# Kernel optimization log

Hardware: AMD Instinct MI355X
Metric: run time of the kernel (lower is better)

Reference implementation:

```python
import jax, jax.numpy as jnp
import numpy as np

D_K = 1024
HEADS = 16
HK = 64
HV = 64


def setup_inputs() -> dict:
    key = jax.random.key(0)
    ks = jax.random.split(key, 12)
    B, S = 4, 2048
    sc_in = 1.0 / np.sqrt(D_K)
    sc_u = 1.0 / np.sqrt(HV * HEADS)
    return {
        "q": jax.random.normal(ks[0], (B, S, D_K), jnp.float32),
        "k": jax.random.normal(ks[1], (B, S, D_K), jnp.float32),
        "v": jax.random.normal(ks[2], (B, S, D_K), jnp.float32),
        "Wq": jax.random.normal(ks[3], (D_K, HK * HEADS), jnp.float32) * sc_in,
        "bq": jax.random.normal(ks[4], (HK * HEADS,), jnp.float32) * sc_in,
        "Wk": jax.random.normal(ks[5], (D_K, HK * HEADS), jnp.float32) * sc_in,
        "bk": jax.random.normal(ks[6], (HK * HEADS,), jnp.float32) * sc_in,
        "Wv": jax.random.normal(ks[7], (D_K, HV * HEADS), jnp.float32) * sc_in,
        "bv": jax.random.normal(ks[8], (HV * HEADS,), jnp.float32) * sc_in,
        "Wu": jax.random.normal(ks[9], (HV * HEADS, D_K), jnp.float32) * sc_u,
        "bu": jax.random.normal(ks[10], (D_K,), jnp.float32) * sc_u,
    }


def reference(q, k, v, Wq, bq, Wk, bk, Wv, bv, Wu, bu):
    B, S, _ = q.shape
    # QKV projections, split heads: (B, S, H, dh) -> (B, H, S, dh)
    qh = (q @ Wq + bq).reshape(B, S, HEADS, HK).transpose(0, 2, 1, 3)
    kh = (k @ Wk + bk).reshape(B, S, HEADS, HK).transpose(0, 2, 1, 3)
    vh = (v @ Wv + bv).reshape(B, S, HEADS, HV).transpose(0, 2, 1, 3)
    # Naive attention: scores scaled by sqrt(head_size) as in Sdpa
    scores = jnp.einsum("bhqd,bhkd->bhqk", qh, kh) / jnp.sqrt(
        jnp.asarray(HK, qh.dtype)
    )
    attn = jax.nn.softmax(scores, axis=-1)
    out = jnp.einsum("bhqk,bhkd->bhqd", attn, vh)  # (B, H, S, HV)
    # Merge heads: (B, S, H*HV), then output projection
    merged = out.transpose(0, 2, 1, 3).reshape(B, S, HEADS * HV)
    return merged @ Wu + bu
```

## Files before the change

### kernel.cpp

```cpp
#include <hip/hip_runtime.h>

typedef __bf16 bf16;
typedef __bf16 bf16x8 __attribute__((ext_vector_type(8)));
typedef __bf16 bf16x4 __attribute__((ext_vector_type(4)));
typedef float  f32x4  __attribute__((ext_vector_type(4)));

#define GLD_LDS16(gp, lp) __builtin_amdgcn_global_load_lds( \
    (const __attribute__((address_space(1))) unsigned int*)(const void*)(gp), \
    (__attribute__((address_space(3))) unsigned int*)(void*)(lp), 16, 0, 0)

constexpr int BB = 4, SSEQ = 2048, DK = 1024, NH = 16, DH = 64;
constexpr int M = BB * SSEQ;

constexpr size_t SZ_X = (size_t)M * DK * 2;
constexpr size_t SZ_W = (size_t)DK * DK * 2;
constexpr size_t OFF_QBF = 0;
constexpr size_t OFF_KBF = OFF_QBF + SZ_X;
constexpr size_t OFF_VBF = OFF_KBF + SZ_X;
constexpr size_t OFF_WQT = OFF_VBF + SZ_X;
constexpr size_t OFF_WKT = OFF_WQT + SZ_W;
constexpr size_t OFF_WVT = OFF_WKT + SZ_W;
constexpr size_t OFF_WUT = OFF_WVT + SZ_W;
constexpr size_t OFF_QH  = OFF_WUT + SZ_W;
constexpr size_t OFF_KH  = OFF_QH + SZ_X;
constexpr size_t OFF_VTH = OFF_KH + SZ_X;
constexpr size_t OFF_MRG = OFF_VTH + SZ_X;

__global__ void cvt_x(const float* __restrict__ q, const float* __restrict__ k,
                      const float* __restrict__ v,
                      bf16* __restrict__ qb, bf16* __restrict__ kb, bf16* __restrict__ vb) {
    const float* s = (blockIdx.z == 0) ? q : (blockIdx.z == 1) ? k : v;
    bf16*        d = (blockIdx.z == 0) ? qb : (blockIdx.z == 1) ? kb : vb;
    size_t i = (size_t)blockIdx.x * blockDim.x + threadIdx.x;
    float4 val = ((const float4*)s)[i];
    bf16x4 o = { (bf16)val.x, (bf16)val.y, (bf16)val.z, (bf16)val.w };
    ((bf16x4*)d)[i] = o;
}

__global__ void cvt_wT(const float* __restrict__ wq, const float* __restrict__ wk,
                       const float* __restrict__ wv, const float* __restrict__ wu,
                       bf16* __restrict__ wqt, bf16* __restrict__ wkt,
                       bf16* __restrict__ wvt, bf16* __restrict__ wut) {
    const float* w = (blockIdx.z == 0) ? wq : (blockIdx.z == 1) ? wk
                   : (blockIdx.z == 2) ? wv : wu;
    bf16* o        = (blockIdx.z == 0) ? wqt : (blockIdx.z == 1) ? wkt
                   : (blockIdx.z == 2) ? wvt : wut;
    __shared__ float t[64][65];
    int tx = threadIdx.x & 63, ty = threadIdx.x >> 6;
    int bx = blockIdx.x * 64, by = blockIdx.y * 64;
#pragma unroll
    for (int r = 0; r < 16; r++) {
        int row = ty * 16 + r;
        t[row][tx] = w[(size_t)(by + row) * DK + bx + tx];
    }
    __syncthreads();
#pragma unroll
    for (int r = 0; r < 16; r++) {
        int row2 = ty * 16 + r;
        o[(size_t)(bx + row2) * DK + by + tx] = (bf16)t[tx][row2];
    }
}

struct GArg {
    const bf16* A; const bf16* BT; const float* bias; void* out; int mode; float oscale;
};

__global__ __launch_bounds__(256, 2) void gemm_bt(GArg g0, GArg g1, GArg g2) {
    GArg g;
    if (blockIdx.z == 0) g = g0; else if (blockIdx.z == 1) g = g1; else g = g2;
    __shared__ __attribute__((aligned(16))) bf16 As[128 * 32];
    __shared__ __attribute__((aligned(16))) bf16 Bs[128 * 32];
    const int tid = threadIdx.x;
    const int lane = tid & 63, wv = tid >> 6;
    const int wm = (wv & 1) * 64, wn = (wv >> 1) * 64;
    const int cl = lane & 15, qd = lane >> 4;
    const int rowbase = blockIdx.y * 128, colbase = blockIdx.x * 128;

    f32x4 acc[4][4];
#pragma unroll
    for (int i = 0; i < 4; i++)
#pragma unroll
        for (int j = 0; j < 4; j++) acc[i][j] = f32x4{0.f, 0.f, 0.f, 0.f};

    for (int k0 = 0; k0 < DK; k0 += 32) {
        __syncthreads();
#pragma unroll
        for (int c = 0; c < 2; c++) {
            int f = (c * 256 + tid) * 8;
            int row = f >> 5, col = f & 31;
            GLD_LDS16(g.A + (size_t)(rowbase + row) * DK + k0 + col, &As[f]);
        }
#pragma unroll
        for (int c = 0; c < 2; c++) {
            int f = (c * 256 + tid) * 8;
            int row = f >> 5, col = f & 31;
            GLD_LDS16(g.BT + (size_t)(colbase + row) * DK + k0 + col, &Bs[f]);
        }
        __syncthreads();
        bf16x8 af[4], bfr[4];
#pragma unroll
        for (int i = 0; i < 4; i++)
            af[i] = *(const bf16x8*)&As[(wm + i * 16 + cl) * 32 + qd * 8];
#pragma unroll
        for (int j = 0; j < 4; j++)
            bfr[j] = *(const bf16x8*)&Bs[(wn + j * 16 + cl) * 32 + qd * 8];
#pragma unroll
        for (int i = 0; i < 4; i++)
#pragma unroll
            for (int j = 0; j < 4; j++)
                acc[i][j] = __builtin_amdgcn_mfma_f32_16x16x32_bf16(af[i], bfr[j], acc[i][j], 0, 0, 0);
    }

    if (g.mode == 2) {
        float* out = (float*)g.out;
#pragma unroll
        for (int i = 0; i < 4; i++)
#pragma unroll
            for (int j = 0; j < 4; j++)
#pragma unroll
                for (int r = 0; r < 4; r++) {
                    int row = rowbase + wm + i * 16 + qd * 4 + r;
                    int col = colbase + wn + j * 16 + cl;
                    out[(size_t)row * DK + col] = (acc[i][j][r] + g.bias[col]) * g.oscale;
                }
    } else if (g.mode == 0) {
        bf16* out = (bf16*)g.out;
#pragma unroll
        for (int i = 0; i < 4; i++)
#pragma unroll
            for (int j = 0; j < 4; j++)
#pragma unroll
                for (int r = 0; r < 4; r++) {
                    int row = rowbase + wm + i * 16 + qd * 4 + r;
                    int col = colbase + wn + j * 16 + cl;
                    int b_ = row >> 11, s_ = row & 2047, h_ = col >> 6, d_ = col & 63;
                    float v = (acc[i][j][r] + g.bias[col]) * g.oscale;
                    out[(((size_t)(b_ * NH + h_)) * SSEQ + s_) * DH + d_] = (bf16)v;
                }
    } else {
        bf16* out = (bf16*)g.out;
#pragma unroll
        for (int i = 0; i < 4; i++)
#pragma unroll
            for (int j = 0; j < 4; j++)
#pragma unroll
                for (int r = 0; r < 4; r++) {
                    int row = rowbase + wm + i * 16 + qd * 4 + r;
                    int col = colbase + wn + j * 16 + cl;
                    int b_ = row >> 11, s_ = row & 2047, h_ = col >> 6, d_ = col & 63;
                    float v = (acc[i][j][r] + g.bias[col]) * g.oscale;
                    out[(((size_t)(b_ * NH + h_)) * DH + d_) * SSEQ + s_] = (bf16)v;
                }
    }
}

__global__ __launch_bounds__(256, 4) void attn(const bf16* __restrict__ Qh,
                                               const bf16* __restrict__ Kh,
                                               const bf16* __restrict__ VTh,
                                               bf16* __restrict__ mrg) {
    __shared__ __attribute__((aligned(16))) bf16 Ks[64 * 64];
    __shared__ __attribute__((aligned(16))) bf16 VTs[64 * 64];
    __shared__ __attribute__((aligned(16))) bf16 Pb[4][32 * 72];
    const int tid = threadIdx.x;
    const int lane = tid & 63, w = tid >> 6;
    const int cl = lane & 15, qd = lane >> 4;
    const int bh = blockIdx.y;
    const int qbase = blockIdx.x * 128;
    const bf16* Qb = Qh + (size_t)bh * SSEQ * DH;
    const bf16* Kb = Kh + (size_t)bh * SSEQ * DH;
    const bf16* Vb = VTh + (size_t)bh * DH * SSEQ;

    bf16x8 qf[2][2];
#pragma unroll
    for (int mi = 0; mi < 2; mi++) {
        int sq = qbase + w * 32 + mi * 16 + cl;
        qf[mi][0] = *(const bf16x8*)&Qb[(size_t)sq * DH + qd * 8];
        qf[mi][1] = *(const bf16x8*)&Qb[(size_t)sq * DH + 32 + qd * 8];
    }
    f32x4 O[2][4];
#pragma unroll
    for (int mi = 0; mi < 2; mi++)
#pragma unroll
        for (int jv = 0; jv < 4; jv++) O[mi][jv] = f32x4{0.f, 0.f, 0.f, 0.f};
    float ps[2][4];
#pragma unroll
    for (int mi = 0; mi < 2; mi++)
#pragma unroll
        for (int r = 0; r < 4; r++) ps[mi][r] = 0.f;

    for (int kt = 0; kt < 32; kt++) {
        const int kbase = kt * 64;
        __syncthreads();
#pragma unroll
        for (int c = 0; c < 2; c++) {
            int L = c * 256 + tid;
            int row = L >> 3, lc = (L & 7) ^ (row & 7);
            GLD_LDS16(Kb + (size_t)(kbase + row) * DH + lc * 8, &Ks[L * 8]);
        }
#pragma unroll
        for (int c = 0; c < 2; c++) {
            int L = c * 256 + tid;
            int row = L >> 3, lc = (L & 7) ^ (row & 7);
            GLD_LDS16(Vb + (size_t)row * SSEQ + kbase + lc * 8, &VTs[L * 8]);
        }
        __syncthreads();

#pragma unroll
        for (int mi = 0; mi < 2; mi++) {
            f32x4 Sc[4];
#pragma unroll
            for (int j = 0; j < 4; j++) Sc[j] = f32x4{0.f, 0.f, 0.f, 0.f};
#pragma unroll
            for (int kc = 0; kc < 2; kc++)
#pragma unroll
                for (int j = 0; j < 4; j++) {
                    bf16x8 bfr = *(const bf16x8*)&Ks[(j * 16 + cl) * 64 + (((kc * 4 + qd) ^ (cl & 7)) * 8)];
                    Sc[j] = __builtin_amdgcn_mfma_f32_16x16x32_bf16(qf[mi][kc], bfr, Sc[j], 0, 0, 0);
                }
#pragma unroll
            for (int j = 0; j < 4; j++)
#pragma unroll
                for (int r = 0; r < 4; r++) {
                    float p = __builtin_amdgcn_exp2f(Sc[j][r]);
                    ps[mi][r] += p;
                    Pb[w][(mi * 16 + qd * 4 + r) * 72 + j * 16 + cl] = (bf16)p;
                }
        }

#pragma unroll
        for (int kc = 0; kc < 2; kc++) {
            bf16x8 vf[4];
#pragma unroll
            for (int jv = 0; jv < 4; jv++)
                vf[jv] = *(const bf16x8*)&VTs[(jv * 16 + cl) * 64 + (((kc * 4 + qd) ^ (cl & 7)) * 8)];
#pragma unroll
            for (int mi = 0; mi < 2; mi++) {
                bf16x8 pf = *(const bf16x8*)&Pb[w][(mi * 16 + cl) * 72 + kc * 32 + qd * 8];
#pragma unroll
                for (int jv = 0; jv < 4; jv++)
                    O[mi][jv] = __builtin_amdgcn_mfma_f32_16x16x32_bf16(pf, vf[jv], O[mi][jv], 0, 0, 0);
            }
        }
    }

    int b_ = bh >> 4, h_ = bh & 15;
#pragma unroll
    for (int mi = 0; mi < 2; mi++)
#pragma unroll
        for (int r = 0; r < 4; r++) {
            float t = ps[mi][r];
#pragma unroll
            for (int off = 1; off < 16; off <<= 1) t += __shfl_xor(t, off);
            float inv = 1.0f / t;
            int sq = qbase + w * 32 + mi * 16 + qd * 4 + r;
            size_t rowoff = ((size_t)(b_ * SSEQ + sq)) * DK + h_ * DH;
#pragma unroll
            for (int jv = 0; jv < 4; jv++)
                mrg[rowoff + jv * 16 + cl] = (bf16)(O[mi][jv][r] * inv);
        }
}

extern "C" void kernel_launch(void* const* d_in, const int* in_sizes, int n_in,
                              void* d_out, int out_size, void* d_ws, size_t ws_size,
                              hipStream_t stream) {
    const float* q  = (const float*)d_in[0];
    const float* k  = (const float*)d_in[1];
    const float* v  = (const float*)d_in[2];
    const float* Wq = (const float*)d_in[3];
    const float* bq = (const float*)d_in[4];
    const float* Wk = (const float*)d_in[5];
    const float* bk = (const float*)d_in[6];
    const float* Wv = (const float*)d_in[7];
    const float* bv = (const float*)d_in[8];
    const float* Wu = (const float*)d_in[9];
    const float* bu = (const float*)d_in[10];
    char* ws = (char*)d_ws;
    bf16* qbf = (bf16*)(ws + OFF_QBF);
    bf16* kbf = (bf16*)(ws + OFF_KBF);
    bf16* vbf = (bf16*)(ws + OFF_VBF);
    bf16* wqt = (bf16*)(ws + OFF_WQT);
    bf16* wkt = (bf16*)(ws + OFF_WKT);
    bf16* wvt = (bf16*)(ws + OFF_WVT);
    bf16* wut = (bf16*)(ws + OFF_WUT);
    bf16* qh  = (bf16*)(ws + OFF_QH);
    bf16* kh  = (bf16*)(ws + OFF_KH);
    bf16* vth = (bf16*)(ws + OFF_VTH);
    bf16* mrg = (bf16*)(ws + OFF_MRG);

    cvt_x<<<dim3(8192, 1, 3), 256, 0, stream>>>(q, k, v, qbf, kbf, vbf);
    cvt_wT<<<dim3(16, 16, 4), 256, 0, stream>>>(Wq, Wk, Wv, Wu, wqt, wkt, wvt, wut);

    GArg gq{qbf, wqt, bq, (void*)qh, 0, 0.18033688011112043f};
    GArg gk{kbf, wkt, bk, (void*)kh, 0, 1.0f};
    GArg gv{vbf, wvt, bv, (void*)vth, 1, 1.0f};
    gemm_bt<<<dim3(8, 64, 3), 256, 0, stream>>>(gq, gk, gv);

    attn<<<dim3(16, 64), 256, 0, stream>>>(qh, kh, vth, mrg);

    GArg go{mrg, wut, bu, d_out, 2, 1.0f};
    gemm_bt<<<dim3(8, 64, 1), 256, 0, stream>>>(go, go, go);
}
```

Baseline: 376.4 us.

## Restructure attention to keep P in registers with double-buffered K/V tiles

The attention kernel now computes S transposed (K as the A operand), so the exponentiated probabilities land in the register layout the PV MFMA (16x16x16) needs, which removes the per-wave LDS round trip for P. Each block handles 256 queries (64 per wave) with double-buffered K/V LDS tiles prefetched one step ahead, and a flat grid remapped so the heads sharing a compute-die group are co-scheduled for L2 reuse. The Q/K projection GEMM writes plain row-major output, and the V projection swaps MFMA operands so the transposed store is more contiguous. In exchange, register pressure rises and occupancy drops to 2 blocks per CU.

```diff
diff --git a/kernel.cpp b/kernel.cpp
--- a/kernel.cpp
+++ b/kernel.cpp
@@ -4,10 +4,16 @@
 typedef __bf16 bf16x8 __attribute__((ext_vector_type(8)));
 typedef __bf16 bf16x4 __attribute__((ext_vector_type(4)));
 typedef float  f32x4  __attribute__((ext_vector_type(4)));
+typedef short  s16x4  __attribute__((ext_vector_type(4)));
 
 #define GLD_LDS16(gp, lp) __builtin_amdgcn_global_load_lds( \
     (const __attribute__((address_space(1))) unsigned int*)(const void*)(gp), \
     (__attribute__((address_space(3))) unsigned int*)(void*)(lp), 16, 0, 0)
+
+static __device__ __forceinline__ f32x4 mfma16(bf16x4 a, bf16x4 b, f32x4 c) {
+    return __builtin_amdgcn_mfma_f32_16x16x16bf16_1k(
+        __builtin_bit_cast(s16x4, a), __builtin_bit_cast(s16x4, b), c, 0, 0, 0);
+}
 
 constexpr int BB = 4, SSEQ = 2048, DK = 1024, NH = 16, DH = 64;
 constexpr int M = BB * SSEQ;
@@ -82,6 +88,7 @@
 #pragma unroll
         for (int j = 0; j < 4; j++) acc[i][j] = f32x4{0.f, 0.f, 0.f, 0.f};
 
+    const bool swapped = (g.mode == 1);
     for (int k0 = 0; k0 < DK; k0 += 32) {
         __syncthreads();
 #pragma unroll
@@ -104,11 +111,19 @@
 #pragma unroll
         for (int j = 0; j < 4; j++)
             bfr[j] = *(const bf16x8*)&Bs[(wn + j * 16 + cl) * 32 + qd * 8];
-#pragma unroll
-        for (int i = 0; i < 4; i++)
-#pragma unroll
-            for (int j = 0; j < 4; j++)
-                acc[i][j] = __builtin_amdgcn_mfma_f32_16x16x32_bf16(af[i], bfr[j], acc[i][j], 0, 0, 0);
+        if (swapped) {
+#pragma unroll
+            for (int i = 0; i < 4; i++)
+#pragma unroll
+                for (int j = 0; j < 4; j++)
+                    acc[i][j] = __builtin_amdgcn_mfma_f32_16x16x32_bf16(bfr[j], af[i], acc[i][j], 0, 0, 0);
+        } else {
+#pragma unroll
+            for (int i = 0; i < 4; i++)
+#pragma unroll
+                for (int j = 0; j < 4; j++)
+                    acc[i][j] = __builtin_amdgcn_mfma_f32_16x16x32_bf16(af[i], bfr[j], acc[i][j], 0, 0, 0);
+        }
     }
 
     if (g.mode == 2) {
@@ -133,9 +148,8 @@
                 for (int r = 0; r < 4; r++) {
                     int row = rowbase + wm + i * 16 + qd * 4 + r;
                     int col = colbase + wn + j * 16 + cl;
-                    int b_ = row >> 11, s_ = row & 2047, h_ = col >> 6, d_ = col & 63;
                     float v = (acc[i][j][r] + g.bias[col]) * g.oscale;
-                    out[(((size_t)(b_ * NH + h_)) * SSEQ + s_) * DH + d_] = (bf16)v;
+                    out[(size_t)row * DK + col] = (bf16)v;
                 }
     } else {
         bf16* out = (bf16*)g.out;
@@ -145,119 +159,121 @@
             for (int j = 0; j < 4; j++)
 #pragma unroll
                 for (int r = 0; r < 4; r++) {
-                    int row = rowbase + wm + i * 16 + qd * 4 + r;
-                    int col = colbase + wn + j * 16 + cl;
-                    int b_ = row >> 11, s_ = row & 2047, h_ = col >> 6, d_ = col & 63;
-                    float v = (acc[i][j][r] + g.bias[col]) * g.oscale;
-                    out[(((size_t)(b_ * NH + h_)) * DH + d_) * SSEQ + s_] = (bf16)v;
+                    int colg = colbase + wn + j * 16 + qd * 4 + r;
+                    int rowg = rowbase + wm + i * 16 + cl;
+                    int b_ = rowg >> 11, s_ = rowg & 2047;
+                    float v = (acc[i][j][r] + g.bias[colg]) * g.oscale;
+                    out[((size_t)(b_ * NH + (colg >> 6)) * DH + (colg & 63)) * SSEQ + s_] = (bf16)v;
                 }
     }
 }
 
-__global__ __launch_bounds__(256, 4) void attn(const bf16* __restrict__ Qh,
+__global__ __launch_bounds__(256, 2) void attn(const bf16* __restrict__ Qh,
                                                const bf16* __restrict__ Kh,
                                                const bf16* __restrict__ VTh,
                                                bf16* __restrict__ mrg) {
-    __shared__ __attribute__((aligned(16))) bf16 Ks[64 * 64];
-    __shared__ __attribute__((aligned(16))) bf16 VTs[64 * 64];
-    __shared__ __attribute__((aligned(16))) bf16 Pb[4][32 * 72];
+    __shared__ __attribute__((aligned(16))) bf16 Ks[2][64 * 64];
+    __shared__ __attribute__((aligned(16))) bf16 VTs[2][64 * 64];
     const int tid = threadIdx.x;
     const int lane = tid & 63, w = tid >> 6;
     const int cl = lane & 15, qd = lane >> 4;
-    const int bh = blockIdx.y;
-    const int qbase = blockIdx.x * 128;
-    const bf16* Qb = Qh + (size_t)bh * SSEQ * DH;
-    const bf16* Kb = Kh + (size_t)bh * SSEQ * DH;
+    const int F = blockIdx.x;
+    const int xcd = F & 7, slot = F >> 3;
+    const int bh = xcd * 8 + (slot & 7);
+    const int qt = slot >> 3;
+    const int b_ = bh >> 4, h_ = bh & 15;
+    const int qbase = qt * 256;
+    const bf16* Qb = Qh + ((size_t)b_ * SSEQ) * DK + h_ * DH;
+    const bf16* Kb = Kh + ((size_t)b_ * SSEQ) * DK + h_ * DH;
     const bf16* Vb = VTh + (size_t)bh * DH * SSEQ;
 
-    bf16x8 qf[2][2];
-#pragma unroll
-    for (int mi = 0; mi < 2; mi++) {
-        int sq = qbase + w * 32 + mi * 16 + cl;
-        qf[mi][0] = *(const bf16x8*)&Qb[(size_t)sq * DH + qd * 8];
-        qf[mi][1] = *(const bf16x8*)&Qb[(size_t)sq * DH + 32 + qd * 8];
-    }
-    f32x4 O[2][4];
-#pragma unroll
-    for (int mi = 0; mi < 2; mi++)
+    bf16x8 qf[4][2];
+#pragma unroll
+    for (int mi = 0; mi < 4; mi++) {
+        int q = qbase + w * 64 + mi * 16 + cl;
+        qf[mi][0] = *(const bf16x8*)&Qb[(size_t)q * DK + qd * 8];
+        qf[mi][1] = *(const bf16x8*)&Qb[(size_t)q * DK + 32 + qd * 8];
+    }
+    f32x4 O[4][4];
+#pragma unroll
+    for (int mi = 0; mi < 4; mi++)
 #pragma unroll
         for (int jv = 0; jv < 4; jv++) O[mi][jv] = f32x4{0.f, 0.f, 0.f, 0.f};
-    float ps[2][4];
-#pragma unroll
-    for (int mi = 0; mi < 2; mi++)
-#pragma unroll
-        for (int r = 0; r < 4; r++) ps[mi][r] = 0.f;
-
-    for (int kt = 0; kt < 32; kt++) {
-        const int kbase = kt * 64;
-        __syncthreads();
+    float ps[4] = {0.f, 0.f, 0.f, 0.f};
+
+    auto stage = [&](int kt, int buf) {
 #pragma unroll
         for (int c = 0; c < 2; c++) {
             int L = c * 256 + tid;
             int row = L >> 3, lc = (L & 7) ^ (row & 7);
-            GLD_LDS16(Kb + (size_t)(kbase + row) * DH + lc * 8, &Ks[L * 8]);
+            GLD_LDS16(Kb + (size_t)(kt * 64 + row) * DK + lc * 8, &Ks[buf][L * 8]);
         }
 #pragma unroll
         for (int c = 0; c < 2; c++) {
             int L = c * 256 + tid;
             int row = L >> 3, lc = (L & 7) ^ (row & 7);
-            GLD_LDS16(Vb + (size_t)row * SSEQ + kbase + lc * 8, &VTs[L * 8]);
-        }
+            GLD_LDS16(Vb + (size_t)row * SSEQ + kt * 64 + lc * 8, &VTs[buf][L * 8]);
+        }
+    };
+    stage(0, 0);
+
+    for (int kt = 0; kt < 32; kt++) {
+        const int buf = kt & 1;
         __syncthreads();
-
-#pragma unroll
-        for (int mi = 0; mi < 2; mi++) {
-            f32x4 Sc[4];
-#pragma unroll
-            for (int j = 0; j < 4; j++) Sc[j] = f32x4{0.f, 0.f, 0.f, 0.f};
-#pragma unroll
-            for (int kc = 0; kc < 2; kc++)
-#pragma unroll
-                for (int j = 0; j < 4; j++) {
-                    bf16x8 bfr = *(const bf16x8*)&Ks[(j * 16 + cl) * 64 + (((kc * 4 + qd) ^ (cl & 7)) * 8)];
-                    Sc[j] = __builtin_amdgcn_mfma_f32_16x16x32_bf16(qf[mi][kc], bfr, Sc[j], 0, 0, 0);
+        if (kt + 1 < 32) stage(kt + 1, buf ^ 1);
+
+        bf16x4 pf[4][4];
+#pragma unroll
+        for (int jt = 0; jt < 4; jt++) {
+            bf16x8 kf0 = *(const bf16x8*)&Ks[buf][(jt * 16 + cl) * 64 + ((qd ^ (cl & 7)) * 8)];
+            bf16x8 kf1 = *(const bf16x8*)&Ks[buf][(jt * 16 + cl) * 64 + (((4 + qd) ^ (cl & 7)) * 8)];
+#pragma unroll
+            for (int mi = 0; mi < 4; mi++) {
+                f32x4 S = __builtin_amdgcn_mfma_f32_16x16x32_bf16(kf0, qf[mi][0],
+                                                                  f32x4{0.f, 0.f, 0.f, 0.f}, 0, 0, 0);
+                S = __builtin_amdgcn_mfma_f32_16x16x32_bf16(kf1, qf[mi][1], S, 0, 0, 0);
+                bf16x4 p4;
+                float s = 0.f;
+#pragma unroll
+                for (int r = 0; r < 4; r++) {
+                    float p = __builtin_amdgcn_exp2f(S[r]);
+                    s += p;
+                    p4[r] = (bf16)p;
                 }
-#pragma unroll
-            for (int j = 0; j < 4; j++)
-#pragma unroll
-                for (int r = 0; r < 4; r++) {
-                    float p = __builtin_amdgcn_exp2f(Sc[j][r]);
-                    ps[mi][r] += p;
-                    Pb[w][(mi * 16 + qd * 4 + r) * 72 + j * 16 + cl] = (bf16)p;
-                }
-        }
-
-#pragma unroll
-        for (int kc = 0; kc < 2; kc++) {
-            bf16x8 vf[4];
-#pragma unroll
-            for (int jv = 0; jv < 4; jv++)
-                vf[jv] = *(const bf16x8*)&VTs[(jv * 16 + cl) * 64 + (((kc * 4 + qd) ^ (cl & 7)) * 8)];
-#pragma unroll
-            for (int mi = 0; mi < 2; mi++) {
-                bf16x8 pf = *(const bf16x8*)&Pb[w][(mi * 16 + cl) * 72 + kc * 32 + qd * 8];
-#pragma unroll
-                for (int jv = 0; jv < 4; jv++)
-                    O[mi][jv] = __builtin_amdgcn_mfma_f32_16x16x32_bf16(pf, vf[jv], O[mi][jv], 0, 0, 0);
+                ps[mi] += s;
+                pf[mi][jt] = p4;
             }
         }
-    }
-
-    int b_ = bh >> 4, h_ = bh & 15;
-#pragma unroll
-    for (int mi = 0; mi < 2; mi++)
-#pragma unroll
-        for (int r = 0; r < 4; r++) {
-            float t = ps[mi][r];
-#pragma unroll
-            for (int off = 1; off < 16; off <<= 1) t += __shfl_xor(t, off);
-            float inv = 1.0f / t;
-            int sq = qbase + w * 32 + mi * 16 + qd * 4 + r;
-            size_t rowoff = ((size_t)(b_ * SSEQ + sq)) * DK + h_ * DH;
-#pragma unroll
-            for (int jv = 0; jv < 4; jv++)
-                mrg[rowoff + jv * 16 + cl] = (bf16)(O[mi][jv][r] * inv);
-        }
+
+#pragma unroll
+        for (int jt = 0; jt < 4; jt++) {
+#pragma unroll
+            for (int jv = 0; jv < 4; jv++) {
+                bf16x4 vf = *(const bf16x4*)&VTs[buf][(jv * 16 + cl) * 64 +
+                                (((jt * 2 + (qd >> 1)) ^ (cl & 7)) * 8) + (qd & 1) * 4];
+#pragma unroll
+                for (int mi = 0; mi < 4; mi++)
+                    O[mi][jv] = mfma16(vf, pf[mi][jt], O[mi][jv]);
+            }
+        }
+    }
+
+#pragma unroll
+    for (int mi = 0; mi < 4; mi++) {
+        float t = ps[mi];
+        t += __shfl_xor(t, 16);
+        t += __shfl_xor(t, 32);
+        float inv = 1.0f / t;
+        int q = qbase + w * 64 + mi * 16 + cl;
+        size_t ro = ((size_t)(b_ * SSEQ + q)) * DK + h_ * DH;
+#pragma unroll
+        for (int jv = 0; jv < 4; jv++) {
+            bf16x4 o4;
+#pragma unroll
+            for (int r = 0; r < 4; r++) o4[r] = (bf16)(O[mi][jv][r] * inv);
+            *(bf16x4*)&mrg[ro + jv * 16 + qd * 4] = o4;
+        }
+    }
 }
 
 extern "C" void kernel_launch(void* const* d_in, const int* in_sizes, int n_in,
@@ -295,7 +311,7 @@
     GArg gv{vbf, wvt, bv, (void*)vth, 1, 1.0f};
     gemm_bt<<<dim3(8, 64, 3), 256, 0, stream>>>(gq, gk, gv);
 
-    attn<<<dim3(16, 64), 256, 0, stream>>>(qh, kh, vth, mrg);
+    attn<<<dim3(512), 256, 0, stream>>>(qh, kh, vth, mrg);
 
     GArg go{mrg, wut, bu, d_out, 2, 1.0f};
     gemm_bt<<<dim3(8, 64, 1), 256, 0, stream>>>(go, go, go);
```

After: 354.9 us. 1.06x faster.
